# Optimization experiments

Measured on AMD Instinct MI355X. Metric: run time of the kernel, lower is better.

Reference implementation:

```python
import jax, jax.numpy as jnp
import numpy as np

NUM_HEADS = 16


def setup_inputs() -> dict:
    key = jax.random.key(0)
    ks = jax.random.split(key, 7)
    B, Lq, Lkv, C, Lpos = 4, 1024, 2048, 1024, 1024
    s = 0.02
    return {
        "q": jax.random.normal(ks[0], (B, Lq, C), jnp.float32),
        "kv": jax.random.normal(ks[1], (B, Lkv, C), jnp.float32),
        "attn_pos": jax.random.normal(ks[2], (B, NUM_HEADS, Lq, Lpos), jnp.float32),
        "q_w": jax.random.normal(ks[3], (C, C), jnp.float32) * s,
        "kv_w": jax.random.normal(ks[4], (2 * C, C), jnp.float32) * s,
        "proj_w": jax.random.normal(ks[5], (C, C), jnp.float32) * s,
        "proj_b": jnp.zeros((C,), jnp.float32),
    }


def reference(q, kv, attn_pos, q_w, kv_w, proj_w, proj_b):
    B, Lq, C = q.shape
    Lkv = kv.shape[1]
    H = NUM_HEADS
    D = C // H
    scale = D ** (-0.5)

    # q projection -> (B, H, Lq, D)
    qh = (q @ q_w.T).reshape(B, Lq, H, D).transpose(0, 2, 1, 3)
    # kv projection -> k, v each (B, H, Lkv, D); torch Linear weight rows: first C -> k, next C -> v
    kvp = kv @ kv_w.T  # (B, Lkv, 2C)
    k = kvp[..., :C].reshape(B, Lkv, H, D).transpose(0, 2, 1, 3)
    v = kvp[..., C:].reshape(B, Lkv, H, D).transpose(0, 2, 1, 3)

    attn = jnp.einsum("bhqd,bhkd->bhqk", qh, k) * scale  # (B, H, Lq, Lkv)
    # zero-pad attn_pos on last dim to Lkv (matches torch cat-with-zeros)
    pad = Lkv - attn_pos.shape[-1]
    if pad > 0:
        attn_pos = jnp.pad(attn_pos, ((0, 0), (0, 0), (0, 0), (0, pad)))
    attn = jax.nn.softmax(attn + attn_pos, axis=-1)

    x = jnp.einsum("bhqk,bhkd->bhqd", attn, v)  # (B, H, Lq, D)
    x = x.transpose(0, 2, 1, 3).reshape(B, Lq, C)
    return x @ proj_w.T + proj_b
```

## Files before the change

kernel.cpp:

```cpp
#include <hip/hip_runtime.h>

using half_t = _Float16;
using half8  = __attribute__((ext_vector_type(8))) _Float16;
using half4  = __attribute__((ext_vector_type(4))) _Float16;
using f32x4  = __attribute__((ext_vector_type(4))) float;

#define MFMA(a, b, c) __builtin_amdgcn_mfma_f32_16x16x32_f16((a), (b), (c), 0, 0, 0)

#define GLL16(g, l)                                                     \
  __builtin_amdgcn_global_load_lds(                                     \
      (__attribute__((address_space(1))) void*)(g),                     \
      (__attribute__((address_space(3))) void*)(l), 16, 0, 0)

__device__ __forceinline__ half8 ld8(const half_t* p) { return *(const half8*)p; }

__global__ void cvt_f32_f16(const float* __restrict__ src, half_t* __restrict__ dst, int n4) {
  int i = blockIdx.x * blockDim.x + threadIdx.x;
  if (i < n4) {
    f32x4 v = ((const f32x4*)src)[i];
    half4 h;
    h[0] = (half_t)v[0]; h[1] = (half_t)v[1]; h[2] = (half_t)v[2]; h[3] = (half_t)v[3];
    ((half4*)dst)[i] = h;
  }
}

template <int EPI>
__global__ __launch_bounds__(256) void gemm_kernel(
    const half_t* __restrict__ A, const half_t* __restrict__ Bt,
    int M, int N, int K,
    half_t* __restrict__ oh, half_t* __restrict__ ov,
    float* __restrict__ of, const float* __restrict__ bias) {
  __shared__ alignas(16) half_t sA[128 * 32];
  __shared__ alignas(16) half_t sB[128 * 32];
  const int tid  = threadIdx.x;
  const int lane = tid & 63;
  const int w    = tid >> 6;
  const int c    = lane & 15;
  const int quad = lane >> 4;
  const int m0 = blockIdx.y * 128;
  const int n0 = blockIdx.x * 128;
  const int wm = (w & 1) * 64;
  const int wn = (w >> 1) * 64;

  f32x4 acc[4][4] = {};

  const int srow = tid >> 2;
  const int scol = (tid & 3) * 8;
  const half_t* Ag = A + (size_t)(m0 + srow) * K + scol;
  const half_t* Bg = Bt + (size_t)(n0 + srow) * K + scol;

  for (int k0 = 0; k0 < K; k0 += 32) {
    GLL16(Ag + k0,            sA + tid * 8);
    GLL16(Ag + k0 + 64 * K,   sA + tid * 8 + 2048);
    GLL16(Bg + k0,            sB + tid * 8);
    GLL16(Bg + k0 + 64 * K,   sB + tid * 8 + 2048);
    __syncthreads();
    half8 a[4], b[4];
#pragma unroll
    for (int i = 0; i < 4; ++i) a[i] = ld8(&sA[(wm + i * 16 + c) * 32 + quad * 8]);
#pragma unroll
    for (int j = 0; j < 4; ++j) b[j] = ld8(&sB[(wn + j * 16 + c) * 32 + quad * 8]);
#pragma unroll
    for (int i = 0; i < 4; ++i)
#pragma unroll
      for (int j = 0; j < 4; ++j) acc[i][j] = MFMA(a[i], b[j], acc[i][j]);
    __syncthreads();
  }

#pragma unroll
  for (int i = 0; i < 4; ++i) {
    const int mbase = m0 + wm + i * 16 + quad * 4;
#pragma unroll
    for (int j = 0; j < 4; ++j) {
      const int n = n0 + wn + j * 16 + c;
      if (EPI == 0) {
        const int bb = mbase >> 10, qi = mbase & 1023;
        const int hh = n >> 6, d = n & 63;
        half_t* p = oh + (((size_t)(bb * 16 + hh) * 1024 + qi) * 64 + d);
#pragma unroll
        for (int r = 0; r < 4; ++r) p[(size_t)r * 64] = (half_t)acc[i][j][r];
      } else if (EPI == 1) {
        const int bb = mbase >> 11, kvi = mbase & 2047;
        if (n < 1024) {
          const int hh = n >> 6, d = n & 63;
          half_t* p = oh + (((size_t)(bb * 16 + hh) * 2048 + kvi) * 64 + d);
#pragma unroll
          for (int r = 0; r < 4; ++r) p[(size_t)r * 64] = (half_t)acc[i][j][r];
        } else {
          const int nn = n - 1024;
          const int hh = nn >> 6, d = nn & 63;
          half4 hv;
#pragma unroll
          for (int r = 0; r < 4; ++r) hv[r] = (half_t)acc[i][j][r];
          *(half4*)&ov[((size_t)(bb * 16 + hh) * 64 + d) * 2048 + kvi] = hv;
        }
      } else {
        const float bv = bias[n];
#pragma unroll
        for (int r = 0; r < 4; ++r) of[(size_t)(mbase + r) * N + n] = acc[i][j][r] + bv;
      }
    }
  }
}

__global__ __launch_bounds__(256) void attn_kernel(
    const half_t* __restrict__ qh, const half_t* __restrict__ kk,
    const half_t* __restrict__ vt, const float* __restrict__ pos,
    half_t* __restrict__ xout) {
  __shared__ alignas(16) half_t Qs[64 * 72];
  __shared__ alignas(16) half_t Ks[64 * 72];
  __shared__ alignas(16) half_t Vs[64 * 72];
  __shared__ alignas(16) half_t Ps[4 * 16 * 72];
  const int tid  = threadIdx.x;
  const int lane = tid & 63;
  const int w    = tid >> 6;
  const int c    = lane & 15;
  const int quad = lane >> 4;
  const int bh = blockIdx.x >> 4;
  const int q0 = (blockIdx.x & 15) << 6;
  const int b  = bh >> 4;
  const int h  = bh & 15;
  const float LOG2E = 1.4426950408889634f;

  {
    const half_t* qg = qh + (((size_t)bh << 10) + q0) * 64;
#pragma unroll
    for (int r2 = 0; r2 < 2; ++r2) {
      const int off = tid * 8 + r2 * 2048;
      const int row = off >> 6, col = off & 63;
      *(half8*)&Qs[row * 72 + col] = *(const half8*)&qg[row * 64 + col];
    }
  }

  f32x4 o[4] = {};
  float m_run[4] = {-1e30f, -1e30f, -1e30f, -1e30f};
  float l_run[4] = {0.f, 0.f, 0.f, 0.f};

  const half_t* kg = kk + ((size_t)bh * 2048) * 64;
  const half_t* vg = vt + ((size_t)bh * 64) * 2048;
  const float*  pg = pos + (((size_t)bh << 10) + q0 + w * 16) * 1024;
  half_t* Pw = Ps + w * 16 * 72;

  for (int kv0 = 0; kv0 < 2048; kv0 += 64) {
    __syncthreads();
#pragma unroll
    for (int r2 = 0; r2 < 2; ++r2) {
      const int off = tid * 8 + r2 * 2048;
      const int row = off >> 6, col = off & 63;
      *(half8*)&Ks[row * 72 + col] = *(const half8*)&kg[(size_t)(kv0 + row) * 64 + col];
      *(half8*)&Vs[row * 72 + col] = *(const half8*)&vg[(size_t)row * 2048 + kv0 + col];
    }
    __syncthreads();

    const half8 aq0 = ld8(&Qs[(w * 16 + c) * 72 + quad * 8]);
    const half8 aq1 = ld8(&Qs[(w * 16 + c) * 72 + 32 + quad * 8]);
    f32x4 s[4];
#pragma unroll
    for (int t = 0; t < 4; ++t) {
      const half8 bk0 = ld8(&Ks[(t * 16 + c) * 72 + quad * 8]);
      const half8 bk1 = ld8(&Ks[(t * 16 + c) * 72 + 32 + quad * 8]);
      f32x4 z = {};
      z = MFMA(aq0, bk0, z);
      z = MFMA(aq1, bk1, z);
      s[t] = z;
    }

    float lg[4][4];
    if (kv0 < 1024) {
#pragma unroll
      for (int t = 0; t < 4; ++t)
#pragma unroll
        for (int r = 0; r < 4; ++r)
          lg[t][r] = s[t][r] * 0.125f + pg[(size_t)(quad * 4 + r) * 1024 + kv0 + t * 16 + c];
    } else {
#pragma unroll
      for (int t = 0; t < 4; ++t)
#pragma unroll
        for (int r = 0; r < 4; ++r) lg[t][r] = s[t][r] * 0.125f;
    }

    float pvv[4][4];
#pragma unroll
    for (int r = 0; r < 4; ++r) {
      float mx = fmaxf(fmaxf(lg[0][r], lg[1][r]), fmaxf(lg[2][r], lg[3][r]));
      mx = fmaxf(mx, __shfl_xor(mx, 1, 16));
      mx = fmaxf(mx, __shfl_xor(mx, 2, 16));
      mx = fmaxf(mx, __shfl_xor(mx, 4, 16));
      mx = fmaxf(mx, __shfl_xor(mx, 8, 16));
      const float mnew  = fmaxf(m_run[r], mx);
      const float alpha = exp2f((m_run[r] - mnew) * LOG2E);
      float rs = 0.f;
#pragma unroll
      for (int t = 0; t < 4; ++t) {
        const float p = exp2f((lg[t][r] - mnew) * LOG2E);
        pvv[t][r] = p;
        rs += p;
      }
      rs += __shfl_xor(rs, 1, 16);
      rs += __shfl_xor(rs, 2, 16);
      rs += __shfl_xor(rs, 4, 16);
      rs += __shfl_xor(rs, 8, 16);
      l_run[r] = l_run[r] * alpha + rs;
      m_run[r] = mnew;
#pragma unroll
      for (int jd = 0; jd < 4; ++jd) o[jd][r] *= alpha;
    }

#pragma unroll
    for (int t = 0; t < 4; ++t)
#pragma unroll
      for (int r = 0; r < 4; ++r)
        Pw[(quad * 4 + r) * 72 + t * 16 + c] = (half_t)pvv[t][r];
    __syncthreads();

#pragma unroll
    for (int hk = 0; hk < 2; ++hk) {
      const half8 ap = ld8(&Pw[c * 72 + hk * 32 + quad * 8]);
#pragma unroll
      for (int jd = 0; jd < 4; ++jd) {
        const half8 bv = ld8(&Vs[(jd * 16 + c) * 72 + hk * 32 + quad * 8]);
        o[jd] = MFMA(ap, bv, o[jd]);
      }
    }
  }

#pragma unroll
  for (int jd = 0; jd < 4; ++jd)
#pragma unroll
    for (int r = 0; r < 4; ++r) {
      const int qrow = q0 + w * 16 + quad * 4 + r;
      const int d    = jd * 16 + c;
      xout[((size_t)b * 1024 + qrow) * 1024 + h * 64 + d] = (half_t)(o[jd][r] / l_run[r]);
    }
}

extern "C" void kernel_launch(void* const* d_in, const int* in_sizes, int n_in,
                              void* d_out, int out_size, void* d_ws, size_t ws_size,
                              hipStream_t stream) {
  const float* q   = (const float*)d_in[0];
  const float* kv  = (const float*)d_in[1];
  const float* pos = (const float*)d_in[2];
  const float* qw  = (const float*)d_in[3];
  const float* kvw = (const float*)d_in[4];
  const float* pw  = (const float*)d_in[5];
  const float* pb  = (const float*)d_in[6];
  float* out = (float*)d_out;

  char* ws = (char*)d_ws;
  half_t* qf   = (half_t*)(ws);
  half_t* kvf  = (half_t*)(ws + (size_t)(8)  * 1048576);
  half_t* qwf  = (half_t*)(ws + (size_t)(24) * 1048576);
  half_t* kvwf = (half_t*)(ws + (size_t)(26) * 1048576);
  half_t* pwf  = (half_t*)(ws + (size_t)(30) * 1048576);
  half_t* qh   = (half_t*)(ws + (size_t)(32) * 1048576);
  half_t* kk   = (half_t*)(ws + (size_t)(40) * 1048576);
  half_t* vt   = (half_t*)(ws + (size_t)(56) * 1048576);
  half_t* xb   = (half_t*)(ws + (size_t)(72) * 1048576);

  auto cvt = [&](const float* s, half_t* d, int n) {
    cvt_f32_f16<<<n / 1024, 256, 0, stream>>>(s, d, n / 4);
  };
  cvt(q,   qf,   4 * 1024 * 1024);
  cvt(kv,  kvf,  4 * 2048 * 1024);
  cvt(qw,  qwf,  1024 * 1024);
  cvt(kvw, kvwf, 2048 * 1024);
  cvt(pw,  pwf,  1024 * 1024);

  gemm_kernel<0><<<dim3(1024 / 128, 4096 / 128), 256, 0, stream>>>(
      qf, qwf, 4096, 1024, 1024, qh, nullptr, nullptr, nullptr);
  gemm_kernel<1><<<dim3(2048 / 128, 8192 / 128), 256, 0, stream>>>(
      kvf, kvwf, 8192, 2048, 1024, kk, vt, nullptr, nullptr);
  attn_kernel<<<4 * 16 * 16, 256, 0, stream>>>(qh, kk, vt, pos, xb);
  gemm_kernel<2><<<dim3(1024 / 128, 4096 / 128), 256, 0, stream>>>(
      xb, pwf, 4096, 1024, 1024, nullptr, nullptr, out, pb);
}
```

Before: 618.9 us.

## Restructure attention kernel with 32x32 MFMA, double-buffered async LDS staging

Rewrites the attention kernel so each wave handles 32 query rows using 32x32x16 MFMAs, with Q held in registers. K, V and the positional bias tiles are double-buffered into swizzled LDS through global_load_lds, so the next tile's loads overlap the current tile's compute. The P matrix is passed between lanes with shuffles instead of an LDS round trip, and the softmax rescale is skipped when no row maximum changes. This targets global-load latency, LDS bank conflicts and per-iteration synchronisation, at the cost of higher register pressure and a halved grid of 1024 blocks.

New measurement: 602.7 us. 1.03x faster.

```diff
diff --git a/kernel.cpp b/kernel.cpp
--- a/kernel.cpp
+++ b/kernel.cpp
@@ -3,9 +3,12 @@
 using half_t = _Float16;
 using half8  = __attribute__((ext_vector_type(8))) _Float16;
 using half4  = __attribute__((ext_vector_type(4))) _Float16;
+using half2v = __attribute__((ext_vector_type(2))) _Float16;
 using f32x4  = __attribute__((ext_vector_type(4))) float;
-
-#define MFMA(a, b, c) __builtin_amdgcn_mfma_f32_16x16x32_f16((a), (b), (c), 0, 0, 0)
+using f32x16 = __attribute__((ext_vector_type(16))) float;
+
+#define MFMA(a, b, c)   __builtin_amdgcn_mfma_f32_16x16x32_f16((a), (b), (c), 0, 0, 0)
+#define MFMA32(a, b, c) __builtin_amdgcn_mfma_f32_32x32x16_f16((a), (b), (c), 0, 0, 0)
 
 #define GLL16(g, l)                                                     \
   __builtin_amdgcn_global_load_lds(                                     \
@@ -103,135 +106,155 @@
   }
 }
 
-__global__ __launch_bounds__(256) void attn_kernel(
+__global__ __launch_bounds__(256, 2) void attn_kernel(
     const half_t* __restrict__ qh, const half_t* __restrict__ kk,
     const half_t* __restrict__ vt, const float* __restrict__ pos,
     half_t* __restrict__ xout) {
-  __shared__ alignas(16) half_t Qs[64 * 72];
-  __shared__ alignas(16) half_t Ks[64 * 72];
-  __shared__ alignas(16) half_t Vs[64 * 72];
-  __shared__ alignas(16) half_t Ps[4 * 16 * 72];
+  __shared__ alignas(16) unsigned char smem[2][24576];
+
   const int tid  = threadIdx.x;
   const int lane = tid & 63;
   const int w    = tid >> 6;
-  const int c    = lane & 15;
-  const int quad = lane >> 4;
-  const int bh = blockIdx.x >> 4;
-  const int q0 = (blockIdx.x & 15) << 6;
-  const int b  = bh >> 4;
-  const int h  = bh & 15;
+  const int lr   = lane & 31;
+  const int hi   = lane >> 5;
+
+  const int bh  = blockIdx.x >> 3;
+  const int q0b = (blockIdx.x & 7) * 128;
+  const int q0w = q0b + w * 32;
+
+  const char* kgb = (const char*)(kk + (size_t)bh * 2048 * 64);
+  const char* vgb = (const char*)(vt + (size_t)bh * 64 * 2048);
+  const char* pgb = (const char*)(pos + ((size_t)bh * 1024 + q0b) * 1024);
+
+  const int krow = tid >> 3;
+  const int kcsw = ((tid & 7) * 16) ^ ((krow & 7) << 4);
+  const int vrow = tid >> 2;
+  const int vcsw = ((tid & 3) * 16) ^ ((vrow & 3) << 4);
+
+  half8 qf[4];
+  {
+    const half_t* qg = qh + ((size_t)bh * 1024 + q0w + lr) * 64 + hi * 8;
+#pragma unroll
+    for (int ks = 0; ks < 4; ++ks) qf[ks] = ld8(qg + ks * 16);
+  }
+
+  f32x16 oa0 = {}, oa1 = {};
+  float m_run = -1e30f, l_run = 0.f;
+
   const float LOG2E = 1.4426950408889634f;
-
-  {
-    const half_t* qg = qh + (((size_t)bh << 10) + q0) * 64;
-#pragma unroll
-    for (int r2 = 0; r2 < 2; ++r2) {
-      const int off = tid * 8 + r2 * 2048;
-      const int row = off >> 6, col = off & 63;
-      *(half8*)&Qs[row * 72 + col] = *(const half8*)&qg[row * 64 + col];
-    }
-  }
-
-  f32x4 o[4] = {};
-  float m_run[4] = {-1e30f, -1e30f, -1e30f, -1e30f};
-  float l_run[4] = {0.f, 0.f, 0.f, 0.f};
-
-  const half_t* kg = kk + ((size_t)bh * 2048) * 64;
-  const half_t* vg = vt + ((size_t)bh * 64) * 2048;
-  const float*  pg = pos + (((size_t)bh << 10) + q0 + w * 16) * 1024;
-  half_t* Pw = Ps + w * 16 * 72;
-
-  for (int kv0 = 0; kv0 < 2048; kv0 += 64) {
+  const float SCL2E = 0.125f * 1.4426950408889634f;
+  const int   kswz  = (lr & 7) << 4;
+  const int   vswz  = (lr & 3) << 4;
+
+  auto stage = [&](int buf, int kv0) {
+    unsigned char* s = smem[buf];
+    GLL16(kgb + (size_t)(kv0 + krow) * 128 + kcsw, s + tid * 16);
+    GLL16(vgb + (size_t)vrow * 4096 + (size_t)kv0 * 2 + vcsw, s + 4096 + tid * 16);
+    if (kv0 < 1024) {
+#pragma unroll
+      for (int i = 0; i < 4; ++i) {
+        const int off  = (i * 256 + tid) * 16;
+        const int prow = off >> 7;
+        const int pc   = (off & 127) ^ ((prow & 7) << 4);
+        GLL16(pgb + (size_t)prow * 4096 + (size_t)kv0 * 4 + pc, s + 8192 + off);
+      }
+    }
+  };
+
+  stage(0, 0);
+  __syncthreads();
+
+  for (int kv0 = 0; kv0 < 2048; kv0 += 32) {
+    const int cur = (kv0 >> 5) & 1;
+    const unsigned char* sb = smem[cur];
+    if (kv0 + 32 < 2048) stage(cur ^ 1, kv0 + 32);
+
+    f32x16 sreg = {};
+#pragma unroll
+    for (int ks = 0; ks < 4; ++ks) {
+      const half8 kf = *(const half8*)(sb + lr * 128 + ((ks * 32 + hi * 16) ^ kswz));
+      sreg = MFMA32(kf, qf[ks], sreg);
+    }
+
+    float lg[16];
+    if (kv0 < 1024) {
+      const unsigned char* sp = sb + 8192 + (size_t)(w * 32 + lr) * 128;
+#pragma unroll
+      for (int t = 0; t < 4; ++t) {
+        const f32x4 pv = *(const f32x4*)(sp + ((t * 32 + hi * 16) ^ kswz));
+#pragma unroll
+        for (int u = 0; u < 4; ++u) lg[t * 4 + u] = sreg[t * 4 + u] * SCL2E + pv[u] * LOG2E;
+      }
+    } else {
+#pragma unroll
+      for (int r = 0; r < 16; ++r) lg[r] = sreg[r] * SCL2E;
+    }
+
+    float mx = lg[0];
+#pragma unroll
+    for (int r = 1; r < 16; ++r) mx = fmaxf(mx, lg[r]);
+    mx = fmaxf(mx, __shfl_xor(mx, 32));
+    if (__any(mx > m_run)) {
+      const float mnew  = fmaxf(m_run, mx);
+      const float alpha = exp2f(m_run - mnew);
+#pragma unroll
+      for (int r = 0; r < 16; ++r) { oa0[r] *= alpha; oa1[r] *= alpha; }
+      l_run *= alpha;
+      m_run = mnew;
+    }
+    float pe[16];
+    float rs = 0.f;
+#pragma unroll
+    for (int r = 0; r < 16; ++r) { pe[r] = exp2f(lg[r] - m_run); rs += pe[r]; }
+    rs += __shfl_xor(rs, 32);
+    l_run += rs;
+
+    unsigned int pk[8], xp[8];
+#pragma unroll
+    for (int e = 0; e < 8; ++e) {
+      union { half2v h; unsigned int u; } cv;
+      cv.h[0] = (half_t)pe[2 * e];
+      cv.h[1] = (half_t)pe[2 * e + 1];
+      pk[e] = cv.u;
+    }
+#pragma unroll
+    for (int e = 0; e < 8; ++e) xp[e] = (unsigned int)__shfl_xor((int)pk[e], 32);
+
+    union { unsigned int u[4]; half8 h; } bf0, bf1;
+    if (hi) {
+      bf0.u[0] = xp[2]; bf0.u[1] = xp[3]; bf0.u[2] = pk[2]; bf0.u[3] = pk[3];
+      bf1.u[0] = xp[6]; bf1.u[1] = xp[7]; bf1.u[2] = pk[6]; bf1.u[3] = pk[7];
+    } else {
+      bf0.u[0] = pk[0]; bf0.u[1] = pk[1]; bf0.u[2] = xp[0]; bf0.u[3] = xp[1];
+      bf1.u[0] = pk[4]; bf1.u[1] = pk[5]; bf1.u[2] = xp[4]; bf1.u[3] = xp[5];
+    }
+
+#pragma unroll
+    for (int m = 0; m < 2; ++m) {
+      const int co = (m * 32 + hi * 16) ^ vswz;
+      const half8 vf0 = *(const half8*)(sb + 4096 + lr * 64 + co);
+      const half8 vf1 = *(const half8*)(sb + 4096 + (32 + lr) * 64 + co);
+      const half8 pb  = m ? bf1.h : bf0.h;
+      oa0 = MFMA32(vf0, pb, oa0);
+      oa1 = MFMA32(vf1, pb, oa1);
+    }
+
     __syncthreads();
-#pragma unroll
-    for (int r2 = 0; r2 < 2; ++r2) {
-      const int off = tid * 8 + r2 * 2048;
-      const int row = off >> 6, col = off & 63;
-      *(half8*)&Ks[row * 72 + col] = *(const half8*)&kg[(size_t)(kv0 + row) * 64 + col];
-      *(half8*)&Vs[row * 72 + col] = *(const half8*)&vg[(size_t)row * 2048 + kv0 + col];
-    }
-    __syncthreads();
-
-    const half8 aq0 = ld8(&Qs[(w * 16 + c) * 72 + quad * 8]);
-    const half8 aq1 = ld8(&Qs[(w * 16 + c) * 72 + 32 + quad * 8]);
-    f32x4 s[4];
-#pragma unroll
-    for (int t = 0; t < 4; ++t) {
-      const half8 bk0 = ld8(&Ks[(t * 16 + c) * 72 + quad * 8]);
-      const half8 bk1 = ld8(&Ks[(t * 16 + c) * 72 + 32 + quad * 8]);
-      f32x4 z = {};
-      z = MFMA(aq0, bk0, z);
-      z = MFMA(aq1, bk1, z);
-      s[t] = z;
-    }
-
-    float lg[4][4];
-    if (kv0 < 1024) {
-#pragma unroll
-      for (int t = 0; t < 4; ++t)
-#pragma unroll
-        for (int r = 0; r < 4; ++r)
-          lg[t][r] = s[t][r] * 0.125f + pg[(size_t)(quad * 4 + r) * 1024 + kv0 + t * 16 + c];
-    } else {
-#pragma unroll
-      for (int t = 0; t < 4; ++t)
-#pragma unroll
-        for (int r = 0; r < 4; ++r) lg[t][r] = s[t][r] * 0.125f;
-    }
-
-    float pvv[4][4];
-#pragma unroll
-    for (int r = 0; r < 4; ++r) {
-      float mx = fmaxf(fmaxf(lg[0][r], lg[1][r]), fmaxf(lg[2][r], lg[3][r]));
-      mx = fmaxf(mx, __shfl_xor(mx, 1, 16));
-      mx = fmaxf(mx, __shfl_xor(mx, 2, 16));
-      mx = fmaxf(mx, __shfl_xor(mx, 4, 16));
-      mx = fmaxf(mx, __shfl_xor(mx, 8, 16));
-      const float mnew  = fmaxf(m_run[r], mx);
-      const float alpha = exp2f((m_run[r] - mnew) * LOG2E);
-      float rs = 0.f;
-#pragma unroll
-      for (int t = 0; t < 4; ++t) {
-        const float p = exp2f((lg[t][r] - mnew) * LOG2E);
-        pvv[t][r] = p;
-        rs += p;
-      }
-      rs += __shfl_xor(rs, 1, 16);
-      rs += __shfl_xor(rs, 2, 16);
-      rs += __shfl_xor(rs, 4, 16);
-      rs += __shfl_xor(rs, 8, 16);
-      l_run[r] = l_run[r] * alpha + rs;
-      m_run[r] = mnew;
-#pragma unroll
-      for (int jd = 0; jd < 4; ++jd) o[jd][r] *= alpha;
-    }
-
-#pragma unroll
-    for (int t = 0; t < 4; ++t)
-#pragma unroll
-      for (int r = 0; r < 4; ++r)
-        Pw[(quad * 4 + r) * 72 + t * 16 + c] = (half_t)pvv[t][r];
-    __syncthreads();
-
-#pragma unroll
-    for (int hk = 0; hk < 2; ++hk) {
-      const half8 ap = ld8(&Pw[c * 72 + hk * 32 + quad * 8]);
-#pragma unroll
-      for (int jd = 0; jd < 4; ++jd) {
-        const half8 bv = ld8(&Vs[(jd * 16 + c) * 72 + hk * 32 + quad * 8]);
-        o[jd] = MFMA(ap, bv, o[jd]);
-      }
-    }
-  }
-
-#pragma unroll
-  for (int jd = 0; jd < 4; ++jd)
-#pragma unroll
-    for (int r = 0; r < 4; ++r) {
-      const int qrow = q0 + w * 16 + quad * 4 + r;
-      const int d    = jd * 16 + c;
-      xout[((size_t)b * 1024 + qrow) * 1024 + h * 64 + d] = (half_t)(o[jd][r] / l_run[r]);
-    }
+  }
+
+  const float inv = 1.0f / l_run;
+  half_t* xg = xout + ((size_t)(bh >> 4) * 1024 + q0w + lr) * 1024 + (bh & 15) * 64;
+#pragma unroll
+  for (int t = 0; t < 4; ++t) {
+    half4 h0, h1;
+#pragma unroll
+    for (int u = 0; u < 4; ++u) {
+      h0[u] = (half_t)(oa0[t * 4 + u] * inv);
+      h1[u] = (half_t)(oa1[t * 4 + u] * inv);
+    }
+    *(half4*)(xg + t * 8 + hi * 4)      = h0;
+    *(half4*)(xg + 32 + t * 8 + hi * 4) = h1;
+  }
 }
 
 extern "C" void kernel_launch(void* const* d_in, const int* in_sizes, int n_in,
@@ -270,7 +293,7 @@
       qf, qwf, 4096, 1024, 1024, qh, nullptr, nullptr, nullptr);
   gemm_kernel<1><<<dim3(2048 / 128, 8192 / 128), 256, 0, stream>>>(
       kvf, kvwf, 8192, 2048, 1024, kk, vt, nullptr, nullptr);
-  attn_kernel<<<4 * 16 * 16, 256, 0, stream>>>(qh, kk, vt, pos, xb);
+  attn_kernel<<<4 * 16 * 8, 256, 0, stream>>>(qh, kk, vt, pos, xb);
   gemm_kernel<2><<<dim3(1024 / 128, 4096 / 128), 256, 0, stream>>>(
       xb, pwf, 4096, 1024, 1024, nullptr, nullptr, out, pb);
 }
```
